# Performance work log

Measured on AMD Instinct MI355X. Metric: run time of the kernel, lower is better.

## Reference

```python
import jax, jax.numpy as jnp
import numpy as np

HIDDEN = 768
E_ROUTED = 32
K_ACT = 4
E_SHARED = 8
RANK = 64
FFN_ROUTED = HIDDEN * 2
FFN_SHARED = HIDDEN * 3


def setup_inputs() -> dict:
    key = jax.random.key(0)
    ks = jax.random.split(key, 8)
    s = 0.02
    return {
        "x": jax.random.normal(ks[0], (2, 2048, HIDDEN), dtype=jnp.float32),
        # shared experts: SwiGLU (gate, up, down), stacked over experts
        "shared_wg": jax.random.normal(ks[1], (E_SHARED, HIDDEN, FFN_SHARED), dtype=jnp.float32) * s,
        "shared_wu": jax.random.normal(ks[2], (E_SHARED, HIDDEN, FFN_SHARED), dtype=jnp.float32) * s,
        "shared_wd": jax.random.normal(ks[3], (E_SHARED, FFN_SHARED, HIDDEN), dtype=jnp.float32) * s,
        # routed experts: Linear -> GELU -> Linear, stacked
        "routed_w1": jax.random.normal(ks[4], (E_ROUTED, HIDDEN, FFN_ROUTED), dtype=jnp.float32) * s,
        "routed_w2": jax.random.normal(ks[5], (E_ROUTED, FFN_ROUTED, HIDDEN), dtype=jnp.float32) * s,
        # low-rank router
        "router_down": jax.random.normal(ks[6], (HIDDEN, RANK), dtype=jnp.float32) * s,
        "router_up": jax.random.normal(ks[7], (RANK, E_ROUTED), dtype=jnp.float32) * s,
    }


def reference(x, shared_wg, shared_wu, shared_wd, routed_w1, routed_w2, router_down, router_up):
    B, S, D = x.shape
    xf = x.reshape(-1, D)  # [T, D]

    # shared experts (SwiGLU), averaged
    g = jnp.einsum('td,edh->eth', xf, shared_wg)
    u = jnp.einsum('td,edh->eth', xf, shared_wu)
    sh = jnp.einsum('eth,ehd->etd', jax.nn.silu(g) * u, shared_wd)
    shared_output = sh.mean(axis=0)  # [T, D] (sum / num_shared_expert)

    # low-rank router + top-k
    router_logits = (xf @ router_down) @ router_up  # [T, E]
    routing_weights, selected = jax.lax.top_k(router_logits, K_ACT)  # [T, K]
    routing_weights = jax.nn.softmax(routing_weights, axis=-1)

    # dense all-expert FFN (faithful to source), then gather top-k (== one-hot einsum)
    h = jnp.einsum('td,edh->eth', xf, routed_w1)
    expert_outputs = jnp.einsum('eth,ehd->etd', jax.nn.gelu(h, approximate=False), routed_w2)  # [E,T,D]
    sel_out = jnp.take_along_axis(expert_outputs.transpose(1, 0, 2), selected[:, :, None], axis=1)  # [T,K,D]
    routed_output = jnp.einsum('tkd,tk->td', sel_out, routing_weights)

    output = (shared_output + routed_output).reshape(B, S, D)

    # aux losses
    counts = jnp.bincount(selected.reshape(-1), length=E_ROUTED).astype(jnp.float32)
    load_balance_loss = jnp.var(counts, ddof=1)  # torch .var() is unbiased
    probs = jax.nn.softmax(router_logits, axis=-1)
    router_entropy = -(probs * jnp.log(probs + 1e-10)).sum(-1).mean()
    shared_norm = jnp.linalg.norm(shared_output, axis=-1).mean()
    routed_norm = jnp.linalg.norm(routed_output, axis=-1).mean()
    balance_loss = jnp.abs(shared_norm - routed_norm)

    return output, load_balance_loss, router_entropy, balance_loss
```

## Files before the change

### kernel.cpp

```cpp
#include <hip/hip_runtime.h>
#include <hip/hip_bf16.h>
#include <math.h>


#define T_TOK 4096
#define DHID 768
#define NE_R 32
#define NE_S 8
#define F_S 2304
#define F_R 1536
#define MAXROWS 20480
#define MAX_TILES 160

typedef float f32x4 __attribute__((ext_vector_type(4)));
typedef short s16x8 __attribute__((ext_vector_type(8)));

__device__ __forceinline__ short f2bf(float f) {
  union { float f; unsigned u; } v; v.f = f;
  unsigned r = v.u + 0x7fffu + ((v.u >> 16) & 1u);
  return (short)(r >> 16);
}

#define GLD16(gsrc, ldst)                                                     \
  __builtin_amdgcn_global_load_lds(                                           \
      (const __attribute__((address_space(1))) void*)(gsrc),                  \
      (__attribute__((address_space(3))) void*)(ldst), 16, 0, 0)

__global__ __launch_bounds__(256) void cvt_x_kernel(const float* __restrict__ in,
                                                    short* __restrict__ out, int n4) {
  int i = blockIdx.x * 256 + threadIdx.x;
  if (i >= n4) return;
  float4 v = ((const float4*)in)[i];
  short4 o;
  o.x = f2bf(v.x); o.y = f2bf(v.y); o.z = f2bf(v.z); o.w = f2bf(v.w);
  ((short4*)out)[i] = o;
}

__global__ __launch_bounds__(256) void transpose_cvt(const float* __restrict__ in,
                                                     short* __restrict__ out,
                                                     int R, int C, long ldo, long out_bstride) {
  __shared__ float tile[32][33];
  int b = blockIdx.z;
  in += (size_t)b * R * C;
  out += (size_t)b * out_bstride;
  int c0 = blockIdx.x * 32, r0 = blockIdx.y * 32;
  int tx = threadIdx.x, ty = threadIdx.y;
#pragma unroll
  for (int i = 0; i < 32; i += 8)
    tile[ty + i][tx] = in[(size_t)(r0 + ty + i) * C + (c0 + tx)];
  __syncthreads();
#pragma unroll
  for (int i = 0; i < 32; i += 8)
    out[(size_t)(c0 + ty + i) * ldo + (r0 + tx)] = f2bf(tile[tx][ty + i]);
}

__global__ __launch_bounds__(64) void router_kernel(const float* __restrict__ x,
    const float* __restrict__ rdown, const float* __restrict__ rup,
    int* __restrict__ sel, float* __restrict__ w4, int* __restrict__ counts,
    float* __restrict__ pent) {
  int t = blockIdx.x;
  int lane = threadIdx.x;
  __shared__ float xs[DHID];
  __shared__ float xrs[64];
  __shared__ float lg[32];
  const float* xt = x + (size_t)t * DHID;
  for (int i = lane; i < DHID; i += 64) xs[i] = xt[i];
  __syncthreads();
  float acc = 0.f;
#pragma unroll 8
  for (int d = 0; d < DHID; ++d) acc += xs[d] * rdown[d * 64 + lane];
  xrs[lane] = acc;
  __syncthreads();
  if (lane < 32) {
    float l = 0.f;
#pragma unroll 8
    for (int r = 0; r < 64; ++r) l += xrs[r] * rup[r * 32 + lane];
    lg[lane] = l;
  }
  __syncthreads();
  if (lane == 0) {
    int si[4]; float sv[4];
    unsigned taken = 0;
    for (int k = 0; k < 4; ++k) {
      float best = -3.4e38f; int bi = 0;
      for (int e = 0; e < 32; ++e)
        if (!((taken >> e) & 1u) && lg[e] > best) { best = lg[e]; bi = e; }
      taken |= 1u << bi; si[k] = bi; sv[k] = best;
    }
    float m = sv[0];
    float wv[4]; float zs = 0.f;
    for (int k = 0; k < 4; ++k) { wv[k] = __expf(sv[k] - m); zs += wv[k]; }
    for (int k = 0; k < 4; ++k) {
      sel[t * 4 + k] = si[k];
      w4[t * 4 + k] = wv[k] / zs;
      atomicAdd(&counts[si[k]], 1);
    }
    float Z = 0.f;
    for (int e = 0; e < 32; ++e) Z += __expf(lg[e] - m);
    float ent = 0.f;
    for (int e = 0; e < 32; ++e) {
      float p = __expf(lg[e] - m) / Z;
      ent -= p * logf(p + 1e-10f);
    }
    pent[t] = ent;
  }
}

__global__ void zero_kernel(int* __restrict__ tlist, float* __restrict__ wslot,
                            int* __restrict__ counts, int* __restrict__ cursor) {
  int i = blockIdx.x * 256 + threadIdx.x;
  if (i < MAXROWS) { tlist[i] = 0; wslot[i] = 0.f; }
  if (i < 32) { counts[i] = 0; cursor[i] = 0; }
}

__global__ void meta_kernel(const int* __restrict__ counts, int* __restrict__ meta) {
  if (threadIdx.x == 0) {
    int acc = 0;
    for (int e = 0; e < 32; ++e) { meta[e] = acc; acc += (counts[e] + 127) >> 7; }
    meta[32] = acc;
  }
}

__global__ __launch_bounds__(256) void build_kernel(const int* __restrict__ sel,
    const float* __restrict__ w4, const int* __restrict__ meta, int* __restrict__ cursor,
    int* __restrict__ tlist, float* __restrict__ wslot, int* __restrict__ pos) {
  int t = blockIdx.x * 256 + threadIdx.x;
  if (t >= T_TOK) return;
#pragma unroll
  for (int k = 0; k < 4; ++k) {
    int e = sel[t * 4 + k];
    int slot = atomicAdd(&cursor[e], 1);
    int g = meta[e] * 128 + slot;
    tlist[g] = t; wslot[g] = w4[t * 4 + k]; pos[t * 4 + k] = g;
  }
}

template<int MODE>
__global__ __launch_bounds__(256, MODE == 0 ? 2 : 1) void gemm_k(
    const short* __restrict__ A, const short* __restrict__ B, const short* __restrict__ B2,
    short* __restrict__ outH, float* __restrict__ outF, const float* __restrict__ wslot,
    const int* __restrict__ meta, const int* __restrict__ tlist,
    int K, int lda, long zbstride, long ldo, long ocolz, long orowz, long acolz) {
  constexpr int BM = 128, BN = 128;
  constexpr int WM = 64, WN = 64, FM = 4, FN = 4;
  __shared__ short As[BM * 64];
  __shared__ short Bs[BN * 64];
  __shared__ short Bs2[(MODE == 0) ? BN * 64 : 64];

  int tid = threadIdx.x;
  int wv = tid >> 6, lane = tid & 63;
  int wr = wv >> 1, wc = wv & 1;
  int lrow = lane & 15, kg = lane >> 4;
  int lrow7 = lrow & 7;
  int z = blockIdx.z;
  int n0 = blockIdx.x * BN;

  int eidx = z;
  int g0 = 0, m0 = blockIdx.y * BM;
  if constexpr (MODE == 1 || MODE == 3) {
    int total = meta[32];
    int ty = blockIdx.y;
    if (ty >= total) return;
    int e = 0;
    while (meta[e + 1] <= ty) ++e;
    eidx = e;
    g0 = ty * BM;
  }

  const short* Bb = B + (size_t)eidx * zbstride + (size_t)n0 * K;
  const short* B2b = (MODE == 0) ? (B2 + (size_t)eidx * zbstride + (size_t)n0 * K) : B;

  int srow = tid >> 3;
  int scol = ((tid & 7) ^ (srow & 7)) * 8;

  const short* asrc[2][2];
  const short* bsrc[4];
  const short* b2src[4];
#pragma unroll
  for (int r = 0; r < 4; ++r) {
    int row = r * 32 + srow;
    const short* ap;
    if constexpr (MODE == 1) {
      int t0 = tlist[g0 + row];
      ap = A + (size_t)t0 * lda + scol;
    } else {
      size_t base_row = (size_t)((MODE == 3) ? g0 : m0) + row;
      ap = A + base_row * lda + (MODE == 2 ? (size_t)acolz * z : 0) + scol;
    }
    asrc[r >> 1][r & 1] = ap;
    bsrc[r] = Bb + (size_t)row * K + scol;
    if constexpr (MODE == 0) b2src[r] = B2b + (size_t)row * K + scol;
  }

  f32x4 acc[FM][FN] = {};
  f32x4 acc2[(MODE == 0) ? FM : 1][(MODE == 0) ? FN : 1] = {};

  for (int kt = 0; kt < K; kt += 64) {
#pragma unroll
    for (int r = 0; r < 4; ++r) {
      GLD16(asrc[r >> 1][r & 1] + kt, As + (r * 32 + wv * 8) * 64);
      GLD16(bsrc[r] + kt, Bs + (r * 32 + wv * 8) * 64);
      if constexpr (MODE == 0)
        GLD16(b2src[r] + kt, Bs2 + (r * 32 + wv * 8) * 64);
    }
    __syncthreads();
#pragma unroll
    for (int ks = 0; ks < 2; ++ks) {
      int pc = ((ks * 4 + kg) ^ lrow7) * 8;
      s16x8 af[FM], bb[FN];
#pragma unroll
      for (int i = 0; i < FM; ++i)
        af[i] = *(const s16x8*)&As[(wr * WM + i * 16 + lrow) * 64 + pc];
#pragma unroll
      for (int j = 0; j < FN; ++j)
        bb[j] = *(const s16x8*)&Bs[(wc * WN + j * 16 + lrow) * 64 + pc];
#pragma unroll
      for (int i = 0; i < FM; ++i)
#pragma unroll
        for (int j = 0; j < FN; ++j)
          acc[i][j] = __builtin_amdgcn_mfma_f32_16x16x32_bf16(af[i], bb[j], acc[i][j], 0, 0, 0);
      if constexpr (MODE == 0) {
        s16x8 b2[FN];
#pragma unroll
        for (int j = 0; j < FN; ++j)
          b2[j] = *(const s16x8*)&Bs2[(wc * WN + j * 16 + lrow) * 64 + pc];
#pragma unroll
        for (int i = 0; i < FM; ++i)
#pragma unroll
          for (int j = 0; j < FN; ++j)
            acc2[i][j] = __builtin_amdgcn_mfma_f32_16x16x32_bf16(af[i], b2[j], acc2[i][j], 0, 0, 0);
      }
    }
    __syncthreads();
  }
#pragma unroll
  for (int i = 0; i < FM; ++i) {
#pragma unroll
    for (int r = 0; r < 4; ++r) {
      int rl = wr * WM + i * 16 + kg * 4 + r;
      float wsc = 0.f;
      if constexpr (MODE == 1) wsc = wslot[g0 + rl];
#pragma unroll
      for (int j = 0; j < FN; ++j) {
        int col = n0 + wc * WN + j * 16 + lrow;
        float v = acc[i][j][r];
        if constexpr (MODE == 0) {
          float u = acc2[i][j][r];
          float h = v / (1.f + __expf(-v)) * u;
          outH[(size_t)(m0 + rl) * ldo + (size_t)z * ocolz + col] = f2bf(h);
        } else if constexpr (MODE == 1) {
          float h = 0.5f * v * (1.f + erff(v * 0.70710678118f)) * wsc;
          outH[(size_t)(g0 + rl) * ldo + col] = f2bf(h);
        } else if constexpr (MODE == 2) {
          outF[(size_t)z * orowz + (size_t)(m0 + rl) * DHID + col] = v;
        } else {
          outF[(size_t)(g0 + rl) * DHID + col] = v;
        }
      }
    }
  }
}

__global__ __launch_bounds__(256) void combine_kernel(const float* __restrict__ spart,
    const float* __restrict__ Y, const int* __restrict__ pos,
    float* __restrict__ out, float* __restrict__ pnorm) {
  int t = blockIdx.x, tid = threadIdx.x;
  int p0 = pos[t * 4], p1 = pos[t * 4 + 1], p2 = pos[t * 4 + 2], p3 = pos[t * 4 + 3];
  size_t base = (size_t)t * DHID;
  float s2 = 0.f, r2 = 0.f;
  for (int d = tid; d < DHID; d += 256) {
    float s = 0.f;
#pragma unroll
    for (int e = 0; e < 8; ++e) s += spart[(size_t)e * T_TOK * DHID + base + d];
    s *= 0.125f;
    float r = Y[(size_t)p0 * DHID + d] + Y[(size_t)p1 * DHID + d] +
              Y[(size_t)p2 * DHID + d] + Y[(size_t)p3 * DHID + d];
    out[base + d] = s + r;
    s2 += s * s; r2 += r * r;
  }
  for (int o = 32; o > 0; o >>= 1) { s2 += __shfl_down(s2, o); r2 += __shfl_down(r2, o); }
  __shared__ float red[8];
  int wv = tid >> 6, lane = tid & 63;
  if (lane == 0) { red[wv] = s2; red[4 + wv] = r2; }
  __syncthreads();
  if (tid == 0) {
    float st = red[0] + red[1] + red[2] + red[3];
    float rt = red[4] + red[5] + red[6] + red[7];
    pnorm[t] = sqrtf(st);
    pnorm[T_TOK + t] = sqrtf(rt);
  }
}

__global__ __launch_bounds__(256) void finalize_kernel(const int* __restrict__ counts,
    const float* __restrict__ pent, const float* __restrict__ pnorm, float* __restrict__ o) {
  int tid = threadIdx.x;
  float es = 0.f, ss = 0.f, rs = 0.f;
  for (int i = tid; i < T_TOK; i += 256) {
    es += pent[i]; ss += pnorm[i]; rs += pnorm[T_TOK + i];
  }
  float vs = 0.f;
  if (tid < 32) { float d = (float)counts[tid] - 512.f; vs = d * d; }
  for (int off = 32; off > 0; off >>= 1) {
    es += __shfl_down(es, off); ss += __shfl_down(ss, off);
    rs += __shfl_down(rs, off); vs += __shfl_down(vs, off);
  }
  __shared__ float red[16];
  int wv = tid >> 6, lane = tid & 63;
  if (lane == 0) { red[wv] = es; red[4 + wv] = ss; red[8 + wv] = rs; red[12 + wv] = vs; }
  __syncthreads();
  if (tid == 0) {
    es = red[0] + red[1] + red[2] + red[3];
    ss = red[4] + red[5] + red[6] + red[7];
    rs = red[8] + red[9] + red[10] + red[11];
    vs = red[12] + red[13] + red[14] + red[15];
    o[0] = vs / 31.f;
    o[1] = es / (float)T_TOK;
    o[2] = fabsf(ss - rs) / (float)T_TOK;
  }
}

extern "C" void kernel_launch(void* const* d_in, const int* in_sizes, int n_in,
                              void* d_out, int out_size, void* d_ws, size_t ws_size,
                              hipStream_t stream) {
  const float* x   = (const float*)d_in[0];
  const float* swg = (const float*)d_in[1];
  const float* swu = (const float*)d_in[2];
  const float* swd = (const float*)d_in[3];
  const float* rw1 = (const float*)d_in[4];
  const float* rw2 = (const float*)d_in[5];
  const float* rdn = (const float*)d_in[6];
  const float* rup = (const float*)d_in[7];
  float* fout = (float*)d_out;

  char* w = (char*)d_ws;
  size_t off = 0;
  auto take = [&](size_t bytes) { char* p = w + off; off = (off + bytes + 255) & ~(size_t)255; return p; };
  short* xbf   = (short*)take((size_t)T_TOK * DHID * 2);
  int*   sel   = (int*)  take((size_t)T_TOK * 4 * 4);
  float* w4    = (float*)take((size_t)T_TOK * 4 * 4);
  int*   pos   = (int*)  take((size_t)T_TOK * 4 * 4);
  int*   counts= (int*)  take(32 * 4);
  int*   cursor= (int*)  take(32 * 4);
  int*   meta  = (int*)  take(64 * 4);
  int*   tlist = (int*)  take((size_t)MAXROWS * 4);
  float* wslot = (float*)take((size_t)MAXROWS * 4);
  float* pent  = (float*)take((size_t)T_TOK * 4);
  float* pnorm = (float*)take((size_t)2 * T_TOK * 4);
  float* spart = (float*)take((size_t)NE_S * T_TOK * DHID * 4);
  char*  arena = w + off;

  short* wgT = (short*)arena;
  short* wuT = wgT + (size_t)NE_S * F_S * DHID;
  short* wdT = wuT + (size_t)NE_S * F_S * DHID;
  short* Hsh = wdT + (size_t)NE_S * F_S * DHID;
  float* Y   = (float*)arena;
  short* w1T = (short*)(arena + (size_t)MAXROWS * DHID * 4);
  short* w2T = w1T + (size_t)NE_R * F_R * DHID;
  short* Hr  = w2T + (size_t)NE_R * F_R * DHID;

  zero_kernel<<<(MAXROWS + 255) / 256, 256, 0, stream>>>(tlist, wslot, counts, cursor);
  cvt_x_kernel<<<(T_TOK * DHID / 4 + 255) / 256, 256, 0, stream>>>(x, xbf, T_TOK * DHID / 4);
  router_kernel<<<T_TOK, 64, 0, stream>>>(x, rdn, rup, sel, w4, counts, pent);
  meta_kernel<<<1, 64, 0, stream>>>(counts, meta);
  build_kernel<<<T_TOK / 256, 256, 0, stream>>>(sel, w4, meta, cursor, tlist, wslot, pos);

  transpose_cvt<<<dim3(F_S / 32, DHID / 32, NE_S), dim3(32, 8), 0, stream>>>(
      swg, wgT, DHID, F_S, DHID, (long)F_S * DHID);
  transpose_cvt<<<dim3(F_S / 32, DHID / 32, NE_S), dim3(32, 8), 0, stream>>>(
      swu, wuT, DHID, F_S, DHID, (long)F_S * DHID);
  transpose_cvt<<<dim3(DHID / 32, F_S / 32, NE_S), dim3(32, 8), 0, stream>>>(
      swd, wdT, F_S, DHID, (long)F_S, (long)DHID * F_S);
  gemm_k<0><<<dim3(F_S / 128, T_TOK / 128, NE_S), 256, 0, stream>>>(
      xbf, wgT, wuT, Hsh, nullptr, nullptr, nullptr, nullptr,
      DHID, DHID, (long)F_S * DHID, (long)NE_S * F_S, (long)F_S, 0, 0);
  gemm_k<2><<<dim3(DHID / 128, T_TOK / 128, NE_S), 256, 0, stream>>>(
      Hsh, wdT, nullptr, nullptr, spart, nullptr, nullptr, nullptr,
      F_S, NE_S * F_S, (long)DHID * F_S, DHID, 0, (long)T_TOK * DHID, (long)F_S);

  transpose_cvt<<<dim3(F_R / 32, DHID / 32, NE_R), dim3(32, 8), 0, stream>>>(
      rw1, w1T, DHID, F_R, DHID, (long)F_R * DHID);
  transpose_cvt<<<dim3(DHID / 32, F_R / 32, NE_R), dim3(32, 8), 0, stream>>>(
      rw2, w2T, F_R, DHID, (long)F_R, (long)DHID * F_R);
  gemm_k<1><<<dim3(F_R / 128, MAX_TILES, 1), 256, 0, stream>>>(
      xbf, w1T, nullptr, Hr, nullptr, wslot, meta, tlist,
      DHID, DHID, (long)F_R * DHID, (long)F_R, 0, 0, 0);
  gemm_k<3><<<dim3(DHID / 128, MAX_TILES, 1), 256, 0, stream>>>(
      Hr, w2T, nullptr, nullptr, Y, nullptr, meta, tlist,
      F_R, F_R, (long)DHID * F_R, DHID, 0, 0, 0);

  combine_kernel<<<T_TOK, 256, 0, stream>>>(spart, Y, pos, fout, pnorm);
  finalize_kernel<<<1, 256, 0, stream>>>(counts, pent, pnorm, fout + (size_t)T_TOK * DHID);
}
```

Measured before the change: 973.5 us.

## Switch GEMMs to 32x32 MFMA, swizzle tiles, fuse transposes and zeroing

Moves the GEMM inner loop from 16x16x32 to 32x32x16 bf16 MFMA with 2x2 fragments per wave, which cuts LDS fragment reads per MFMA. It also adds a grouped block-index swizzle for the dense shared-expert GEMMs and makes the down-projection handle two experts per block, halving the fp32 partial-sum buffer read by the combine step. The weight transposes are merged into two launches, zeroing is folded into the x conversion, and launch bounds for the non-gate modes are raised to allow more resident blocks. Register pressure and changed occupancy hints may affect performance either way.

```diff
diff --git a/kernel.cpp b/kernel.cpp
--- a/kernel.cpp
+++ b/kernel.cpp
@@ -12,7 +12,7 @@
 #define MAXROWS 20480
 #define MAX_TILES 160
 
-typedef float f32x4 __attribute__((ext_vector_type(4)));
+typedef float f32x16 __attribute__((ext_vector_type(16)));
 typedef short s16x8 __attribute__((ext_vector_type(8)));
 
 __device__ __forceinline__ short f2bf(float f) {
@@ -27,24 +27,58 @@
       (__attribute__((address_space(3))) void*)(ldst), 16, 0, 0)
 
 __global__ __launch_bounds__(256) void cvt_x_kernel(const float* __restrict__ in,
-                                                    short* __restrict__ out, int n4) {
+    short* __restrict__ out, int* __restrict__ tlist, float* __restrict__ wslot,
+    int* __restrict__ counts, int* __restrict__ cursor) {
   int i = blockIdx.x * 256 + threadIdx.x;
-  if (i >= n4) return;
-  float4 v = ((const float4*)in)[i];
-  short4 o;
-  o.x = f2bf(v.x); o.y = f2bf(v.y); o.z = f2bf(v.z); o.w = f2bf(v.w);
-  ((short4*)out)[i] = o;
-}
-
-__global__ __launch_bounds__(256) void transpose_cvt(const float* __restrict__ in,
-                                                     short* __restrict__ out,
-                                                     int R, int C, long ldo, long out_bstride) {
+  if (i < T_TOK * DHID / 4) {
+    float4 v = ((const float4*)in)[i];
+    short4 o;
+    o.x = f2bf(v.x); o.y = f2bf(v.y); o.z = f2bf(v.z); o.w = f2bf(v.w);
+    ((short4*)out)[i] = o;
+  }
+  if (i < MAXROWS) { tlist[i] = 0; wslot[i] = 0.f; }
+  if (i < 32) { counts[i] = 0; cursor[i] = 0; }
+}
+
+__global__ __launch_bounds__(256) void transpose_shared(
+    const float* __restrict__ swg, const float* __restrict__ swu,
+    const float* __restrict__ swd, short* __restrict__ wgT,
+    short* __restrict__ wuT, short* __restrict__ wdT) {
+  int bid = blockIdx.x;
+  const float* in; short* out; int R, C, nbx; long ldo;
+  if (bid < 13824)      { in = swg; out = wgT; R = DHID; C = F_S; ldo = DHID; nbx = 72; }
+  else if (bid < 27648) { bid -= 13824; in = swu; out = wuT; R = DHID; C = F_S; ldo = DHID; nbx = 72; }
+  else                  { bid -= 27648; in = swd; out = wdT; R = F_S; C = DHID; ldo = F_S; nbx = 24; }
+  int per = nbx * (R / 32);
+  int b = bid / per, rem = bid % per;
+  int c0 = (rem % nbx) * 32, r0 = (rem / nbx) * 32;
+  in  += (size_t)b * R * C;
+  out += (size_t)b * R * C;
+  int tx = threadIdx.x & 31, ty = threadIdx.x >> 5;
   __shared__ float tile[32][33];
-  int b = blockIdx.z;
-  in += (size_t)b * R * C;
-  out += (size_t)b * out_bstride;
-  int c0 = blockIdx.x * 32, r0 = blockIdx.y * 32;
-  int tx = threadIdx.x, ty = threadIdx.y;
+#pragma unroll
+  for (int i = 0; i < 32; i += 8)
+    tile[ty + i][tx] = in[(size_t)(r0 + ty + i) * C + (c0 + tx)];
+  __syncthreads();
+#pragma unroll
+  for (int i = 0; i < 32; i += 8)
+    out[(size_t)(c0 + ty + i) * ldo + (r0 + tx)] = f2bf(tile[tx][ty + i]);
+}
+
+__global__ __launch_bounds__(256) void transpose_routed(
+    const float* __restrict__ rw1, const float* __restrict__ rw2,
+    short* __restrict__ w1T, short* __restrict__ w2T) {
+  int bid = blockIdx.x;
+  const float* in; short* out; int R, C, nbx; long ldo;
+  if (bid < 36864) { in = rw1; out = w1T; R = DHID; C = F_R; ldo = DHID; nbx = 48; }
+  else             { bid -= 36864; in = rw2; out = w2T; R = F_R; C = DHID; ldo = F_R; nbx = 24; }
+  int per = nbx * (R / 32);
+  int b = bid / per, rem = bid % per;
+  int c0 = (rem % nbx) * 32, r0 = (rem / nbx) * 32;
+  in  += (size_t)b * R * C;
+  out += (size_t)b * R * C;
+  int tx = threadIdx.x & 31, ty = threadIdx.x >> 5;
+  __shared__ float tile[32][33];
 #pragma unroll
   for (int i = 0; i < 32; i += 8)
     tile[ty + i][tx] = in[(size_t)(r0 + ty + i) * C + (c0 + tx)];
@@ -106,13 +140,6 @@
   }
 }
 
-__global__ void zero_kernel(int* __restrict__ tlist, float* __restrict__ wslot,
-                            int* __restrict__ counts, int* __restrict__ cursor) {
-  int i = blockIdx.x * 256 + threadIdx.x;
-  if (i < MAXROWS) { tlist[i] = 0; wslot[i] = 0.f; }
-  if (i < 32) { counts[i] = 0; cursor[i] = 0; }
-}
-
 __global__ void meta_kernel(const int* __restrict__ counts, int* __restrict__ meta) {
   if (threadIdx.x == 0) {
     int acc = 0;
@@ -136,13 +163,12 @@
 }
 
 template<int MODE>
-__global__ __launch_bounds__(256, MODE == 0 ? 2 : 1) void gemm_k(
+__global__ __launch_bounds__(256, MODE == 0 ? 2 : 3) void gemm_k(
     const short* __restrict__ A, const short* __restrict__ B, const short* __restrict__ B2,
     short* __restrict__ outH, float* __restrict__ outF, const float* __restrict__ wslot,
     const int* __restrict__ meta, const int* __restrict__ tlist,
     int K, int lda, long zbstride, long ldo, long ocolz, long orowz, long acolz) {
   constexpr int BM = 128, BN = 128;
-  constexpr int WM = 64, WN = 64, FM = 4, FN = 4;
   __shared__ short As[BM * 64];
   __shared__ short Bs[BN * 64];
   __shared__ short Bs2[(MODE == 0) ? BN * 64 : 64];
@@ -150,13 +176,21 @@
   int tid = threadIdx.x;
   int wv = tid >> 6, lane = tid & 63;
   int wr = wv >> 1, wc = wv & 1;
-  int lrow = lane & 15, kg = lane >> 4;
-  int lrow7 = lrow & 7;
+  int lr = lane & 31, kh = lane >> 5;
   int z = blockIdx.z;
-  int n0 = blockIdx.x * BN;
+
+  int bx = blockIdx.x, by = blockIdx.y;
+  if constexpr (MODE == 0 || MODE == 2) {
+    int gx = gridDim.x, gy = gridDim.y;
+    int nwg = gx * gy;
+    int orig = by * gx + bx;
+    int swz = (orig & 7) * (nwg >> 3) + (orig >> 3);
+    bx = swz / gy; by = swz % gy;
+  }
+  int n0 = bx * BN;
 
   int eidx = z;
-  int g0 = 0, m0 = blockIdx.y * BM;
+  int g0 = 0, m0 = by * BM;
   if constexpr (MODE == 1 || MODE == 3) {
     int total = meta[32];
     int ty = blockIdx.y;
@@ -167,85 +201,103 @@
     g0 = ty * BM;
   }
 
-  const short* Bb = B + (size_t)eidx * zbstride + (size_t)n0 * K;
-  const short* B2b = (MODE == 0) ? (B2 + (size_t)eidx * zbstride + (size_t)n0 * K) : B;
-
   int srow = tid >> 3;
   int scol = ((tid & 7) ^ (srow & 7)) * 8;
 
-  const short* asrc[2][2];
-  const short* bsrc[4];
-  const short* b2src[4];
-#pragma unroll
-  for (int r = 0; r < 4; ++r) {
-    int row = r * 32 + srow;
-    const short* ap;
-    if constexpr (MODE == 1) {
-      int t0 = tlist[g0 + row];
-      ap = A + (size_t)t0 * lda + scol;
-    } else {
-      size_t base_row = (size_t)((MODE == 3) ? g0 : m0) + row;
-      ap = A + base_row * lda + (MODE == 2 ? (size_t)acolz * z : 0) + scol;
-    }
-    asrc[r >> 1][r & 1] = ap;
-    bsrc[r] = Bb + (size_t)row * K + scol;
-    if constexpr (MODE == 0) b2src[r] = B2b + (size_t)row * K + scol;
-  }
-
-  f32x4 acc[FM][FN] = {};
-  f32x4 acc2[(MODE == 0) ? FM : 1][(MODE == 0) ? FN : 1] = {};
-
-  for (int kt = 0; kt < K; kt += 64) {
-#pragma unroll
-    for (int r = 0; r < 4; ++r) {
-      GLD16(asrc[r >> 1][r & 1] + kt, As + (r * 32 + wv * 8) * 64);
-      GLD16(bsrc[r] + kt, Bs + (r * 32 + wv * 8) * 64);
-      if constexpr (MODE == 0)
-        GLD16(b2src[r] + kt, Bs2 + (r * 32 + wv * 8) * 64);
-    }
-    __syncthreads();
-#pragma unroll
-    for (int ks = 0; ks < 2; ++ks) {
-      int pc = ((ks * 4 + kg) ^ lrow7) * 8;
-      s16x8 af[FM], bb[FN];
-#pragma unroll
-      for (int i = 0; i < FM; ++i)
-        af[i] = *(const s16x8*)&As[(wr * WM + i * 16 + lrow) * 64 + pc];
-#pragma unroll
-      for (int j = 0; j < FN; ++j)
-        bb[j] = *(const s16x8*)&Bs[(wc * WN + j * 16 + lrow) * 64 + pc];
-#pragma unroll
-      for (int i = 0; i < FM; ++i)
-#pragma unroll
-        for (int j = 0; j < FN; ++j)
-          acc[i][j] = __builtin_amdgcn_mfma_f32_16x16x32_bf16(af[i], bb[j], acc[i][j], 0, 0, 0);
+  f32x16 acc[2][2] = {};
+  f32x16 acc2[(MODE == 0) ? 2 : 1][(MODE == 0) ? 2 : 1] = {};
+
+  constexpr int EPB = (MODE == 2) ? 2 : 1;
+#pragma unroll 1
+  for (int ei = 0; ei < EPB; ++ei) {
+    int e = (MODE == 2) ? (z * 2 + ei) : eidx;
+    const short* Bb = B + (size_t)e * zbstride + (size_t)n0 * K;
+    const short* B2b = (MODE == 0) ? (B2 + (size_t)e * zbstride + (size_t)n0 * K) : B;
+
+    const short *as0, *as1, *as2, *as3;
+    {
+      auto arow = [&](int row) -> const short* {
+        if constexpr (MODE == 1) {
+          return A + (size_t)tlist[g0 + row] * lda + scol;
+        } else if constexpr (MODE == 2) {
+          return A + ((size_t)(m0 + row)) * lda + (size_t)e * acolz + scol;
+        } else if constexpr (MODE == 3) {
+          return A + ((size_t)(g0 + row)) * lda + scol;
+        } else {
+          return A + ((size_t)(m0 + row)) * lda + scol;
+        }
+      };
+      as0 = arow(srow); as1 = arow(32 + srow); as2 = arow(64 + srow); as3 = arow(96 + srow);
+    }
+    const short* bs0 = Bb + (size_t)srow * K + scol;
+    const short* bs1 = bs0 + (size_t)32 * K;
+    const short* bs2 = bs0 + (size_t)64 * K;
+    const short* bs3 = bs0 + (size_t)96 * K;
+    const short* c2s0 = B2b + (size_t)srow * K + scol;
+    const short* c2s1 = c2s0 + (size_t)32 * K;
+    const short* c2s2 = c2s0 + (size_t)64 * K;
+    const short* c2s3 = c2s0 + (size_t)96 * K;
+
+    for (int kt = 0; kt < K; kt += 64) {
+      GLD16(as0 + kt, As + (0 * 32 + wv * 8) * 64);
+      GLD16(as1 + kt, As + (1 * 32 + wv * 8) * 64);
+      GLD16(as2 + kt, As + (2 * 32 + wv * 8) * 64);
+      GLD16(as3 + kt, As + (3 * 32 + wv * 8) * 64);
+      GLD16(bs0 + kt, Bs + (0 * 32 + wv * 8) * 64);
+      GLD16(bs1 + kt, Bs + (1 * 32 + wv * 8) * 64);
+      GLD16(bs2 + kt, Bs + (2 * 32 + wv * 8) * 64);
+      GLD16(bs3 + kt, Bs + (3 * 32 + wv * 8) * 64);
       if constexpr (MODE == 0) {
-        s16x8 b2[FN];
-#pragma unroll
-        for (int j = 0; j < FN; ++j)
-          b2[j] = *(const s16x8*)&Bs2[(wc * WN + j * 16 + lrow) * 64 + pc];
-#pragma unroll
-        for (int i = 0; i < FM; ++i)
-#pragma unroll
-          for (int j = 0; j < FN; ++j)
-            acc2[i][j] = __builtin_amdgcn_mfma_f32_16x16x32_bf16(af[i], b2[j], acc2[i][j], 0, 0, 0);
+        GLD16(c2s0 + kt, Bs2 + (0 * 32 + wv * 8) * 64);
+        GLD16(c2s1 + kt, Bs2 + (1 * 32 + wv * 8) * 64);
+        GLD16(c2s2 + kt, Bs2 + (2 * 32 + wv * 8) * 64);
+        GLD16(c2s3 + kt, Bs2 + (3 * 32 + wv * 8) * 64);
       }
-    }
-    __syncthreads();
-  }
-#pragma unroll
-  for (int i = 0; i < FM; ++i) {
-#pragma unroll
-    for (int r = 0; r < 4; ++r) {
-      int rl = wr * WM + i * 16 + kg * 4 + r;
+      __syncthreads();
+#pragma unroll
+      for (int kq = 0; kq < 4; ++kq) {
+        int pc = ((kq * 2 + kh) ^ (lr & 7)) * 8;
+        s16x8 af[2], bb[2];
+#pragma unroll
+        for (int mi = 0; mi < 2; ++mi)
+          af[mi] = *(const s16x8*)&As[(wr * 64 + mi * 32 + lr) * 64 + pc];
+#pragma unroll
+        for (int nj = 0; nj < 2; ++nj)
+          bb[nj] = *(const s16x8*)&Bs[(wc * 64 + nj * 32 + lr) * 64 + pc];
+#pragma unroll
+        for (int mi = 0; mi < 2; ++mi)
+#pragma unroll
+          for (int nj = 0; nj < 2; ++nj)
+            acc[mi][nj] = __builtin_amdgcn_mfma_f32_32x32x16_bf16(af[mi], bb[nj], acc[mi][nj], 0, 0, 0);
+        if constexpr (MODE == 0) {
+          s16x8 b2[2];
+#pragma unroll
+          for (int nj = 0; nj < 2; ++nj)
+            b2[nj] = *(const s16x8*)&Bs2[(wc * 64 + nj * 32 + lr) * 64 + pc];
+#pragma unroll
+          for (int mi = 0; mi < 2; ++mi)
+#pragma unroll
+            for (int nj = 0; nj < 2; ++nj)
+              acc2[mi][nj] = __builtin_amdgcn_mfma_f32_32x32x16_bf16(af[mi], b2[nj], acc2[mi][nj], 0, 0, 0);
+        }
+      }
+      __syncthreads();
+    }
+  }
+
+#pragma unroll
+  for (int mi = 0; mi < 2; ++mi) {
+#pragma unroll
+    for (int rg = 0; rg < 16; ++rg) {
+      int rl = wr * 64 + mi * 32 + (rg & 3) + 8 * (rg >> 2) + 4 * kh;
       float wsc = 0.f;
       if constexpr (MODE == 1) wsc = wslot[g0 + rl];
 #pragma unroll
-      for (int j = 0; j < FN; ++j) {
-        int col = n0 + wc * WN + j * 16 + lrow;
-        float v = acc[i][j][r];
+      for (int nj = 0; nj < 2; ++nj) {
+        int col = n0 + wc * 64 + nj * 32 + lr;
+        float v = acc[mi][nj][rg];
         if constexpr (MODE == 0) {
-          float u = acc2[i][j][r];
+          float u = acc2[mi][nj][rg];
           float h = v / (1.f + __expf(-v)) * u;
           outH[(size_t)(m0 + rl) * ldo + (size_t)z * ocolz + col] = f2bf(h);
         } else if constexpr (MODE == 1) {
@@ -271,7 +323,7 @@
   for (int d = tid; d < DHID; d += 256) {
     float s = 0.f;
 #pragma unroll
-    for (int e = 0; e < 8; ++e) s += spart[(size_t)e * T_TOK * DHID + base + d];
+    for (int e = 0; e < 4; ++e) s += spart[(size_t)e * T_TOK * DHID + base + d];
     s *= 0.125f;
     float r = Y[(size_t)p0 * DHID + d] + Y[(size_t)p1 * DHID + d] +
               Y[(size_t)p2 * DHID + d] + Y[(size_t)p3 * DHID + d];
@@ -346,7 +398,7 @@
   float* wslot = (float*)take((size_t)MAXROWS * 4);
   float* pent  = (float*)take((size_t)T_TOK * 4);
   float* pnorm = (float*)take((size_t)2 * T_TOK * 4);
-  float* spart = (float*)take((size_t)NE_S * T_TOK * DHID * 4);
+  float* spart = (float*)take((size_t)4 * T_TOK * DHID * 4);
   char*  arena = w + off;
 
   short* wgT = (short*)arena;
@@ -358,29 +410,20 @@
   short* w2T = w1T + (size_t)NE_R * F_R * DHID;
   short* Hr  = w2T + (size_t)NE_R * F_R * DHID;
 
-  zero_kernel<<<(MAXROWS + 255) / 256, 256, 0, stream>>>(tlist, wslot, counts, cursor);
-  cvt_x_kernel<<<(T_TOK * DHID / 4 + 255) / 256, 256, 0, stream>>>(x, xbf, T_TOK * DHID / 4);
+  cvt_x_kernel<<<(T_TOK * DHID / 4 + 255) / 256, 256, 0, stream>>>(x, xbf, tlist, wslot, counts, cursor);
   router_kernel<<<T_TOK, 64, 0, stream>>>(x, rdn, rup, sel, w4, counts, pent);
   meta_kernel<<<1, 64, 0, stream>>>(counts, meta);
   build_kernel<<<T_TOK / 256, 256, 0, stream>>>(sel, w4, meta, cursor, tlist, wslot, pos);
 
-  transpose_cvt<<<dim3(F_S / 32, DHID / 32, NE_S), dim3(32, 8), 0, stream>>>(
-      swg, wgT, DHID, F_S, DHID, (long)F_S * DHID);
-  transpose_cvt<<<dim3(F_S / 32, DHID / 32, NE_S), dim3(32, 8), 0, stream>>>(
-      swu, wuT, DHID, F_S, DHID, (long)F_S * DHID);
-  transpose_cvt<<<dim3(DHID / 32, F_S / 32, NE_S), dim3(32, 8), 0, stream>>>(
-      swd, wdT, F_S, DHID, (long)F_S, (long)DHID * F_S);
+  transpose_shared<<<41472, 256, 0, stream>>>(swg, swu, swd, wgT, wuT, wdT);
   gemm_k<0><<<dim3(F_S / 128, T_TOK / 128, NE_S), 256, 0, stream>>>(
       xbf, wgT, wuT, Hsh, nullptr, nullptr, nullptr, nullptr,
       DHID, DHID, (long)F_S * DHID, (long)NE_S * F_S, (long)F_S, 0, 0);
-  gemm_k<2><<<dim3(DHID / 128, T_TOK / 128, NE_S), 256, 0, stream>>>(
+  gemm_k<2><<<dim3(DHID / 128, T_TOK / 128, NE_S / 2), 256, 0, stream>>>(
       Hsh, wdT, nullptr, nullptr, spart, nullptr, nullptr, nullptr,
       F_S, NE_S * F_S, (long)DHID * F_S, DHID, 0, (long)T_TOK * DHID, (long)F_S);
 
-  transpose_cvt<<<dim3(F_R / 32, DHID / 32, NE_R), dim3(32, 8), 0, stream>>>(
-      rw1, w1T, DHID, F_R, DHID, (long)F_R * DHID);
-  transpose_cvt<<<dim3(DHID / 32, F_R / 32, NE_R), dim3(32, 8), 0, stream>>>(
-      rw2, w2T, F_R, DHID, (long)F_R, (long)DHID * F_R);
+  transpose_routed<<<73728, 256, 0, stream>>>(rw1, rw2, w1T, w2T);
   gemm_k<1><<<dim3(F_R / 128, MAX_TILES, 1), 256, 0, stream>>>(
       xbf, w1T, nullptr, Hr, nullptr, wslot, meta, tlist,
       DHID, DHID, (long)F_R * DHID, (long)F_R, 0, 0, 0);
```

Result: faster. 940.5 us (-3.4%).
